# Kernel tuning notes

Hardware: AMD Instinct MI355X
Metric: run time of the kernel (lower is better)

Reference implementation:

```python
import jax, jax.numpy as jnp
import numpy as np

H = 12          # num_attention_heads
DH = 64         # attention_head_size
EPS = 1e-12     # F.normalize eps
MAX_LOG_SCALE = float(np.log(1.0 / 0.01))  # clamp max for logit_scale


def _l2norm(x):
    # F.normalize(x, dim=-1): x / max(||x||_2, eps)
    n = jnp.sqrt(jnp.sum(x * x, axis=-1, keepdims=True))
    return x / jnp.maximum(n, EPS)


def setup_inputs() -> dict:
    key = jax.random.key(0)
    ks = jax.random.split(key, 9)
    B, S, D = 4, 2048, 768
    sd = 1.0 / np.sqrt(D)
    inp = {
        "hidden_states": jax.random.normal(ks[0], (B, S, D), jnp.float32),
        "Wq": jax.random.normal(ks[1], (D, D), jnp.float32) * sd,
        "bq": jnp.zeros((D,), jnp.float32),
        "Wk": jax.random.normal(ks[2], (D, D), jnp.float32) * sd,
        "bk": jnp.zeros((D,), jnp.float32),
        "Wv": jax.random.normal(ks[3], (D, D), jnp.float32) * sd,
        "bv": jnp.zeros((D,), jnp.float32),
        "Wo": jax.random.normal(ks[4], (D, D), jnp.float32) * sd,
        "bo": jnp.zeros((D,), jnp.float32),
        "logit_scale": jnp.log(10.0 * jnp.ones((H, 1, 1), jnp.float32)),
    }
    return inp


def reference(hidden_states, Wq, bq, Wk, bk, Wv, bv, Wo, bo, logit_scale):
    B, S, D = hidden_states.shape
    # QKV projections (torch Linear: x @ W.T + b), split heads -> [B,H,S,DH]
    def proj(W, b):
        y = hidden_states @ W.T + b
        return y.reshape(B, S, H, DH).transpose(0, 2, 1, 3)
    q = proj(Wq, bq)
    k = proj(Wk, bk)
    v = proj(Wv, bv)
    # cosine-similarity scores scaled by clamped-exp per-head logit scale
    scale = jnp.exp(jnp.minimum(logit_scale, MAX_LOG_SCALE))  # [H,1,1]
    scores = jnp.einsum('bhqd,bhkd->bhqk', _l2norm(q), _l2norm(k)) * scale[None]
    probs = jax.nn.softmax(scores, axis=-1)
    ctx = jnp.einsum('bhqk,bhkd->bhqd', probs, v)
    ctx = ctx.transpose(0, 2, 1, 3).reshape(B, S, D)
    return ctx @ Wo.T + bo
```

## Files before the change

kernel.cpp:

```cpp
#include <hip/hip_runtime.h>
#include <math.h>

#define Hh 12
#define S_LEN 2048
#define D_MODEL 768
#define HD 64

static constexpr float MAXLS = 4.6051701859880914f;
static constexpr float LOG2E = 1.4426950408889634f;

typedef short bf16x8 __attribute__((ext_vector_type(8)));
typedef float f32x4  __attribute__((ext_vector_type(4)));
typedef float f32x16 __attribute__((ext_vector_type(16)));
typedef unsigned short u16x4 __attribute__((ext_vector_type(4)));
typedef unsigned short u16x8 __attribute__((ext_vector_type(8)));
typedef unsigned int u32x4 __attribute__((ext_vector_type(4)));

__device__ __forceinline__ unsigned short f2bf(float x) {
    unsigned int u = __builtin_bit_cast(unsigned int, x);
    unsigned int r = (u + 0x7FFF + ((u >> 16) & 1)) >> 16;
    return (unsigned short)r;
}

__device__ __forceinline__ unsigned int cvtpk(float a, float b) {
    unsigned int r;
    asm("v_cvt_pk_bf16_f32 %0, %1, %2" : "=v"(r) : "v"(a), "v"(b));
    return r;
}

__device__ __forceinline__ void gload16(const void* g, void* l) {
    __builtin_amdgcn_global_load_lds(
        (const __attribute__((address_space(1))) unsigned int*)g,
        (__attribute__((address_space(3))) unsigned int*)l, 16, 0, 0);
}

__global__ __launch_bounds__(256)
void convert_bf16(const float* __restrict__ hs,
                  const float* __restrict__ Wq, const float* __restrict__ Wk,
                  const float* __restrict__ Wv, const float* __restrict__ Wo,
                  unsigned short* __restrict__ hsb,
                  unsigned short* __restrict__ wqkvb,
                  unsigned short* __restrict__ wob)
{
    const long long N0 = 8192LL * 768;
    const long long NW = 768LL * 768;
    const long long e  = ((long long)blockIdx.x * 256 + threadIdx.x) * 8;
    const float* src; unsigned short* dst;
    if (e < N0) { src = hs + e; dst = hsb + e; }
    else if (e < N0 + 3*NW) {
        const long long r = e - N0;
        const int z = (int)(r / NW);
        src = (z == 0 ? Wq : z == 1 ? Wk : Wv) + (r - (long long)z * NW);
        dst = wqkvb + r;
    } else {
        const long long r = e - N0 - 3*NW;
        src = Wo + r; dst = wob + r;
    }
    const float4 f0 = *(const float4*)src;
    const float4 f1 = *(const float4*)(src + 4);
    u16x8 o;
    o[0]=f2bf(f0.x); o[1]=f2bf(f0.y); o[2]=f2bf(f0.z); o[3]=f2bf(f0.w);
    o[4]=f2bf(f1.x); o[5]=f2bf(f1.y); o[6]=f2bf(f1.z); o[7]=f2bf(f1.w);
    *(u16x8*)dst = o;
}

template<int MODE>
__global__ __launch_bounds__(256)
void gemm_bf16(const unsigned short* __restrict__ A,
               const unsigned short* __restrict__ Wt,
               const float* __restrict__ b0, const float* __restrict__ b1,
               const float* __restrict__ b2, const float* __restrict__ ls,
               unsigned short* __restrict__ qb, unsigned short* __restrict__ kb,
               unsigned short* __restrict__ vt, float* __restrict__ out)
{
    constexpr int K = 768;
    __shared__ char As[16384];
    __shared__ char Bs[16384];

    const int tid = threadIdx.x, w = tid >> 6, l = tid & 63;
    const int wr = w >> 1, wc = w & 1, hi = l >> 4, ll = l & 15;
    const int n0 = blockIdx.x * 128, m0 = blockIdx.y * 128;

    const int srow = l >> 3;
    const int sch  = (l & 7) ^ srow;
    const char* Ab = (const char*)(A  + (size_t)(m0 + w*32) * K) + srow * (K*2) + sch * 16;
    const char* Bb = (const char*)(Wt + (size_t)(n0 + w*32) * K) + srow * (K*2) + sch * 16;
    char* AsW = As + (w*32) * 128;
    char* BsW = Bs + (w*32) * 128;

    f32x4 acc[4][4];
    #pragma unroll
    for (int i = 0; i < 4; ++i)
        #pragma unroll
        for (int j = 0; j < 4; ++j) acc[i][j] = (f32x4){0.f,0.f,0.f,0.f};

    for (int kt = 0; kt < K/64; ++kt) {
        __syncthreads();
        #pragma unroll
        for (int s = 0; s < 4; ++s) {
            gload16(Ab + kt*128 + s*8*(K*2), AsW + s*1024);
            gload16(Bb + kt*128 + s*8*(K*2), BsW + s*1024);
        }
        __syncthreads();

        bf16x8 af[2][4], bf[2][4];
        #pragma unroll
        for (int kk = 0; kk < 2; ++kk) {
            const int pc = kk*4 + hi;
            #pragma unroll
            for (int i = 0; i < 4; ++i) {
                const int ra = wr*64 + i*16 + ll;
                af[kk][i] = *(const bf16x8*)(As + ra*128 + ((pc ^ (ra & 7)) << 4));
                const int rb = wc*64 + i*16 + ll;
                bf[kk][i] = *(const bf16x8*)(Bs + rb*128 + ((pc ^ (rb & 7)) << 4));
            }
        }
        #pragma unroll
        for (int kk = 0; kk < 2; ++kk)
            #pragma unroll
            for (int i = 0; i < 4; ++i)
                #pragma unroll
                for (int j = 0; j < 4; ++j)
                    acc[i][j] = __builtin_amdgcn_mfma_f32_16x16x32_bf16(af[kk][i], bf[kk][j], acc[i][j], 0, 0, 0);
    }

    if (MODE == 0) {
        const int z  = n0 / 768;
        const int nl = (n0 % 768) + wc*64;
        const int h  = nl >> 6;
        const int b  = m0 >> 11;
        const int s0 = (m0 & (S_LEN-1)) + wr*64;
        const float* bias = (z == 0) ? b0 : (z == 1) ? b1 : b2;
        float bj[4];
        #pragma unroll
        for (int j = 0; j < 4; ++j) bj[j] = bias[nl + j*16 + ll];

        if (z < 2) {
            const float sc = (z == 0) ? expf(fminf(ls[h], MAXLS)) * LOG2E : 1.0f;
            unsigned short* dst = (z == 0 ? qb : kb) + ((size_t)(b*Hh + h) * S_LEN) * HD;
            #pragma unroll
            for (int i = 0; i < 4; ++i) {
                float vv[4][4]; float ss[4] = {0.f, 0.f, 0.f, 0.f};
                #pragma unroll
                for (int r = 0; r < 4; ++r)
                    #pragma unroll
                    for (int j = 0; j < 4; ++j) {
                        const float x = acc[i][j][r] + bj[j];
                        vv[r][j] = x; ss[r] += x * x;
                    }
                #pragma unroll
                for (int mm = 1; mm < 16; mm <<= 1) {
                    ss[0] += __shfl_xor(ss[0], mm, 64);
                    ss[1] += __shfl_xor(ss[1], mm, 64);
                    ss[2] += __shfl_xor(ss[2], mm, 64);
                    ss[3] += __shfl_xor(ss[3], mm, 64);
                }
                #pragma unroll
                for (int r = 0; r < 4; ++r) {
                    const float inv = sc / fmaxf(sqrtf(ss[r]), 1e-12f);
                    const int s = s0 + i*16 + hi*4 + r;
                    u16x4 o;
                    #pragma unroll
                    for (int j = 0; j < 4; ++j) o[j] = f2bf(vv[r][j] * inv);
                    *(u16x4*)(dst + (size_t)s * HD + ll*4) = o;
                }
            }
        } else {
            const int hsw = ((hi & 1) << 1) | (hi >> 1);
            #pragma unroll
            for (int j = 0; j < 4; ++j) {
                const int d = (nl & 63) + j*16 + ll;
                #pragma unroll
                for (int i = 0; i < 4; ++i) {
                    const int s = s0 + i*16 + hsw*4;
                    u16x4 o;
                    #pragma unroll
                    for (int r = 0; r < 4; ++r) o[r] = f2bf(acc[i][j][r] + bj[j]);
                    *(u16x4*)(vt + ((size_t)(b*Hh + h) * HD + d) * S_LEN + s) = o;
                }
            }
        }
    } else {
        #pragma unroll
        for (int i = 0; i < 4; ++i)
            #pragma unroll
            for (int j = 0; j < 4; ++j) {
                const int n = n0 + wc*64 + j*16 + ll;
                const float bn = b0[n];
                #pragma unroll
                for (int r = 0; r < 4; ++r) {
                    const int m = m0 + wr*64 + i*16 + hi*4 + r;
                    out[(size_t)m * D_MODEL + n] = acc[i][j][r] + bn;
                }
            }
    }
}

__global__ __launch_bounds__(256)
void attn_mfma4(const char* __restrict__ qb_, const char* __restrict__ kb_,
                const char* __restrict__ vtb_,
                unsigned short* __restrict__ ctx)
{
    __shared__ char smem[32768];

    const int flat = blockIdx.x;
    const int xcd = flat & 7, ix = flat >> 3;
    const int bh = xcd * 6 + (ix >> 4);
    const int q0 = (ix & 15) * 128;
    const int b = bh / Hh, h = bh % Hh;

    const int tid = threadIdx.x, w = tid >> 6, l = tid & 63;
    const int lq = l & 31, g = l >> 5;

    const char* qg = qb_ + ((size_t)bh * S_LEN + q0 + w * 32) * 128;
    const char* kg = kb_ + (size_t)bh * S_LEN * 128 + (size_t)l * 128;
    const char* vg = vtb_ + (size_t)bh * HD * (S_LEN * 2) + (size_t)l * 4096;

    bf16x8 qf[4];
    #pragma unroll
    for (int s = 0; s < 4; ++s)
        qf[s] = *(const bf16x8*)(qg + lq * 128 + s * 32 + g * 16);

    const short oneb = (short)0x3F80;
    const bf16x8 onesf = {oneb, oneb, oneb, oneb, oneb, oneb, oneb, oneb};

    f32x16 acco0, acco1, accl;
    #pragma unroll
    for (int i = 0; i < 16; ++i) { acco0[i] = 0.f; acco1[i] = 0.f; accl[i] = 0.f; }

#define STAGE(buf, kt) do {                                                  \
        char* dstS = smem + ((buf) << 14);                                   \
        gload16(kg + (size_t)(kt) * 8192 + w * 16,        dstS + w * 1024);          \
        gload16(kg + (size_t)(kt) * 8192 + (w+4) * 16,    dstS + (w+4) * 1024);      \
        gload16(vg + (size_t)(kt) * 128 + w * 16,         dstS + 8192 + w * 1024);   \
        gload16(vg + (size_t)(kt) * 128 + (w+4) * 16,     dstS + 8192 + (w+4) * 1024); \
    } while (0)

    STAGE(0, 0);
    __syncthreads();
    int cur = 0;

    for (int kt = 0; kt < S_LEN / 64; ++kt) {
        if (kt < S_LEN / 64 - 1) STAGE(cur ^ 1, kt + 1);

        const char* Ks = smem + (cur << 14);
        const char* Vs = Ks + 8192;

        f32x16 sa0, sa1;
        #pragma unroll
        for (int i = 0; i < 16; ++i) { sa0[i] = 0.f; sa1[i] = 0.f; }

        __builtin_amdgcn_s_setprio(1);
        #pragma unroll
        for (int s = 0; s < 4; ++s) {
            const bf16x8 kf0 = *(const bf16x8*)(Ks + (2*s + g) * 1024 + lq * 16);
            sa0 = __builtin_amdgcn_mfma_f32_32x32x16_bf16(kf0, qf[s], sa0, 0, 0, 0);
            const bf16x8 kf1 = *(const bf16x8*)(Ks + (2*s + g) * 1024 + 512 + lq * 16);
            sa1 = __builtin_amdgcn_mfma_f32_32x32x16_bf16(kf1, qf[s], sa1, 0, 0, 0);
        }
        __builtin_amdgcn_s_setprio(0);

        #pragma unroll
        for (int t = 0; t < 4; ++t) {
            float p[8];
            #pragma unroll
            for (int e = 0; e < 8; ++e) {
                const float sv = (t & 2) ? sa1[8*(t&1) + e] : sa0[8*(t&1) + e];
                p[e] = __builtin_amdgcn_exp2f(sv);
            }
            u32x4 pu;
            pu[0] = cvtpk(p[0], p[1]);
            pu[1] = cvtpk(p[2], p[3]);
            pu[2] = cvtpk(p[4], p[5]);
            pu[3] = cvtpk(p[6], p[7]);
            const bf16x8 pa = __builtin_bit_cast(bf16x8, pu);

            __builtin_amdgcn_s_setprio(1);
            const bf16x8 vf0 = *(const bf16x8*)(Vs + (2*t + g) * 1024 + lq * 16);
            acco0 = __builtin_amdgcn_mfma_f32_32x32x16_bf16(pa, vf0, acco0, 0, 0, 0);
            const bf16x8 vf1 = *(const bf16x8*)(Vs + (2*t + g) * 1024 + 512 + lq * 16);
            acco1 = __builtin_amdgcn_mfma_f32_32x32x16_bf16(pa, vf1, acco1, 0, 0, 0);
            accl  = __builtin_amdgcn_mfma_f32_32x32x16_bf16(pa, onesf, accl, 0, 0, 0);
            __builtin_amdgcn_s_setprio(0);
        }

        __syncthreads();
        cur ^= 1;
    }
#undef STAGE

    #pragma unroll
    for (int r = 0; r < 16; ++r) {
        const int qrow = (r & 3) + 8 * (r >> 2) + 4 * g;
        const float inv = 1.0f / accl[r];
        unsigned short* crow = ctx + ((size_t)b * S_LEN + q0 + w * 32 + qrow) * D_MODEL + h * HD;
        crow[lq]      = f2bf(acco0[r] * inv);
        crow[32 + lq] = f2bf(acco1[r] * inv);
    }
}

extern "C" void kernel_launch(void* const* d_in, const int* in_sizes, int n_in,
                              void* d_out, int out_size, void* d_ws, size_t ws_size,
                              hipStream_t stream)
{
    const float* hs = (const float*)d_in[0];
    const float* Wq = (const float*)d_in[1];
    const float* bq = (const float*)d_in[2];
    const float* Wk = (const float*)d_in[3];
    const float* bk = (const float*)d_in[4];
    const float* Wv = (const float*)d_in[5];
    const float* bv = (const float*)d_in[6];
    const float* Wo = (const float*)d_in[7];
    const float* bo = (const float*)d_in[8];
    const float* ls = (const float*)d_in[9];
    float* out = (float*)d_out;

    const int B = 4;
    const size_t nHS = 8192ULL * 768;
    const size_t nW  = 768ULL * 768;
    const size_t nPB = (size_t)B * Hh * S_LEN * HD;

    unsigned short* hsb   = (unsigned short*)d_ws;
    unsigned short* wqkvb = hsb + nHS;
    unsigned short* wob   = wqkvb + 3 * nW;
    unsigned short* qbuf  = wob + nW;
    unsigned short* kbuf  = qbuf + nPB;
    unsigned short* vtb   = kbuf + nPB;
    unsigned short* cbuf  = vtb + nPB;

    hipLaunchKernelGGL(convert_bf16, dim3(4224), dim3(256), 0, stream,
                       hs, Wq, Wk, Wv, Wo, hsb, wqkvb, wob);

    hipLaunchKernelGGL((gemm_bf16<0>), dim3(2304/128, 8192/128), dim3(256), 0, stream,
                       hsb, wqkvb, bq, bk, bv, ls, qbuf, kbuf, vtb, nullptr);

    hipLaunchKernelGGL(attn_mfma4, dim3((S_LEN/128) * B * Hh), dim3(256), 0, stream,
                       (const char*)qbuf, (const char*)kbuf, (const char*)vtb, cbuf);

    hipLaunchKernelGGL((gemm_bf16<1>), dim3(768/128, 8192/128), dim3(256), 0, stream,
                       cbuf, wob, bo, nullptr, nullptr, nullptr,
                       nullptr, nullptr, nullptr, out);
}
```

Before: 229.2 us.

## Pipeline attention QK ahead of PV, remap GEMM blocks per XCD, stage V-transpose through LDS

The attention kernel now uses a triple-buffered LDS ring and computes the QK scores for the next tile before the softmax and PV of the current tile, so matrix work can overlap exp and loads. Its launch bounds now request 4 blocks per CU. The GEMMs get a flattened grid with an XCD-aware block remap. The output projection uses a narrower 64-column tile, which gives more blocks. The V-transpose epilogue in the QKV GEMM goes through LDS so it can issue coalesced 16-byte row stores instead of scattered 8-byte stores. These changes add register pressure and LDS use in attention, plus an extra barrier in the GEMM epilogue.

```diff
diff --git a/kernel.cpp b/kernel.cpp
--- a/kernel.cpp
+++ b/kernel.cpp
@@ -64,7 +64,7 @@
     *(u16x8*)dst = o;
 }
 
-template<int MODE>
+template<int MODE, int BN, int NWGX>
 __global__ __launch_bounds__(256)
 void gemm_bf16(const unsigned short* __restrict__ A,
                const unsigned short* __restrict__ Wt,
@@ -73,37 +73,44 @@
                unsigned short* __restrict__ qb, unsigned short* __restrict__ kb,
                unsigned short* __restrict__ vt, float* __restrict__ out)
 {
-    constexpr int K = 768;
+    constexpr int K  = 768;
+    constexpr int JW = BN / 32;
     __shared__ char As[16384];
-    __shared__ char Bs[16384];
+    __shared__ char Bs[BN * 128];
+
+    constexpr int CPX = (NWGX * 64) / 8;
+    const int bid = blockIdx.x;
+    const int wg  = (bid & 7) * CPX + (bid >> 3);
+    const int n0  = (wg % NWGX) * BN;
+    const int m0  = (wg / NWGX) * 128;
 
     const int tid = threadIdx.x, w = tid >> 6, l = tid & 63;
     const int wr = w >> 1, wc = w & 1, hi = l >> 4, ll = l & 15;
-    const int n0 = blockIdx.x * 128, m0 = blockIdx.y * 128;
 
     const int srow = l >> 3;
     const int sch  = (l & 7) ^ srow;
     const char* Ab = (const char*)(A  + (size_t)(m0 + w*32) * K) + srow * (K*2) + sch * 16;
-    const char* Bb = (const char*)(Wt + (size_t)(n0 + w*32) * K) + srow * (K*2) + sch * 16;
+    const char* Bb = (const char*)(Wt + (size_t)(n0 + w*(BN/4)) * K) + srow * (K*2) + sch * 16;
     char* AsW = As + (w*32) * 128;
-    char* BsW = Bs + (w*32) * 128;
-
-    f32x4 acc[4][4];
+    char* BsW = Bs + (w*(BN/4)) * 128;
+
+    f32x4 acc[4][JW];
     #pragma unroll
     for (int i = 0; i < 4; ++i)
         #pragma unroll
-        for (int j = 0; j < 4; ++j) acc[i][j] = (f32x4){0.f,0.f,0.f,0.f};
+        for (int j = 0; j < JW; ++j) acc[i][j] = (f32x4){0.f,0.f,0.f,0.f};
 
     for (int kt = 0; kt < K/64; ++kt) {
         __syncthreads();
         #pragma unroll
-        for (int s = 0; s < 4; ++s) {
+        for (int s = 0; s < 4; ++s)
             gload16(Ab + kt*128 + s*8*(K*2), AsW + s*1024);
+        #pragma unroll
+        for (int s = 0; s < JW; ++s)
             gload16(Bb + kt*128 + s*8*(K*2), BsW + s*1024);
-        }
         __syncthreads();
 
-        bf16x8 af[2][4], bf[2][4];
+        bf16x8 af[2][4], bf[2][JW];
         #pragma unroll
         for (int kk = 0; kk < 2; ++kk) {
             const int pc = kk*4 + hi;
@@ -111,8 +118,11 @@
             for (int i = 0; i < 4; ++i) {
                 const int ra = wr*64 + i*16 + ll;
                 af[kk][i] = *(const bf16x8*)(As + ra*128 + ((pc ^ (ra & 7)) << 4));
-                const int rb = wc*64 + i*16 + ll;
-                bf[kk][i] = *(const bf16x8*)(Bs + rb*128 + ((pc ^ (rb & 7)) << 4));
+            }
+            #pragma unroll
+            for (int j = 0; j < JW; ++j) {
+                const int rb = wc*(BN/2) + j*16 + ll;
+                bf[kk][j] = *(const bf16x8*)(Bs + rb*128 + ((pc ^ (rb & 7)) << 4));
             }
         }
         #pragma unroll
@@ -120,7 +130,7 @@
             #pragma unroll
             for (int i = 0; i < 4; ++i)
                 #pragma unroll
-                for (int j = 0; j < 4; ++j)
+                for (int j = 0; j < JW; ++j)
                     acc[i][j] = __builtin_amdgcn_mfma_f32_16x16x32_bf16(af[kk][i], bf[kk][j], acc[i][j], 0, 0, 0);
     }
 
@@ -166,17 +176,32 @@
                 }
             }
         } else {
-            const int hsw = ((hi & 1) << 1) | (hi >> 1);
+            __syncthreads();
+            char* T = (w < 2 ? As : Bs) + (w & 1) * 8192;
+            const int ch_add = hi & 1;
+            const int half8  = hi >> 1;
             #pragma unroll
             for (int j = 0; j < 4; ++j) {
-                const int d = (nl & 63) + j*16 + ll;
+                const int d = j*16 + ll;
                 #pragma unroll
                 for (int i = 0; i < 4; ++i) {
-                    const int s = s0 + i*16 + hsw*4;
                     u16x4 o;
                     #pragma unroll
                     for (int r = 0; r < 4; ++r) o[r] = f2bf(acc[i][j][r] + bj[j]);
-                    *(u16x4*)(vt + ((size_t)(b*Hh + h) * HD + d) * S_LEN + s) = o;
+                    const int byteoff = d*128 + (((i*2 + ch_add) ^ (d & 7)) << 4) + half8*8;
+                    *(u16x4*)(T + byteoff) = o;
+                }
+            }
+            const int dl = l >> 2;
+            #pragma unroll
+            for (int dp = 0; dp < 4; ++dp) {
+                const int d = dp*16 + dl;
+                unsigned short* vrow = vt + ((size_t)(b*Hh + h) * HD + d) * S_LEN + s0;
+                #pragma unroll
+                for (int rep = 0; rep < 2; ++rep) {
+                    const int c = (l & 3) + rep*4;
+                    const u16x8 vv = *(const u16x8*)(T + d*128 + ((c ^ (d & 7)) << 4));
+                    *(u16x8*)(vrow + c*8) = vv;
                 }
             }
         }
@@ -184,8 +209,8 @@
         #pragma unroll
         for (int i = 0; i < 4; ++i)
             #pragma unroll
-            for (int j = 0; j < 4; ++j) {
-                const int n = n0 + wc*64 + j*16 + ll;
+            for (int j = 0; j < JW; ++j) {
+                const int n = n0 + wc*(BN/2) + j*16 + ll;
                 const float bn = b0[n];
                 #pragma unroll
                 for (int r = 0; r < 4; ++r) {
@@ -196,12 +221,13 @@
     }
 }
 
-__global__ __launch_bounds__(256)
-void attn_mfma4(const char* __restrict__ qb_, const char* __restrict__ kb_,
+__global__ __launch_bounds__(256, 4)
+void attn_mfma5(const char* __restrict__ qb_, const char* __restrict__ kb_,
                 const char* __restrict__ vtb_,
                 unsigned short* __restrict__ ctx)
 {
-    __shared__ char smem[32768];
+    __shared__ char smem[49152];
+    constexpr int NT = S_LEN / 64;
 
     const int flat = blockIdx.x;
     const int xcd = flat & 7, ix = flat >> 3;
@@ -228,44 +254,33 @@
     #pragma unroll
     for (int i = 0; i < 16; ++i) { acco0[i] = 0.f; acco1[i] = 0.f; accl[i] = 0.f; }
 
-#define STAGE(buf, kt) do {                                                  \
-        char* dstS = smem + ((buf) << 14);                                   \
+#define STAGE(bi, kt) do {                                                   \
+        char* dstS = smem + ((bi) << 14);                                    \
         gload16(kg + (size_t)(kt) * 8192 + w * 16,        dstS + w * 1024);          \
         gload16(kg + (size_t)(kt) * 8192 + (w+4) * 16,    dstS + (w+4) * 1024);      \
         gload16(vg + (size_t)(kt) * 128 + w * 16,         dstS + 8192 + w * 1024);   \
         gload16(vg + (size_t)(kt) * 128 + (w+4) * 16,     dstS + 8192 + (w+4) * 1024); \
     } while (0)
 
-    STAGE(0, 0);
-    __syncthreads();
-    int cur = 0;
-
-    for (int kt = 0; kt < S_LEN / 64; ++kt) {
-        if (kt < S_LEN / 64 - 1) STAGE(cur ^ 1, kt + 1);
-
-        const char* Ks = smem + (cur << 14);
-        const char* Vs = Ks + 8192;
-
-        f32x16 sa0, sa1;
-        #pragma unroll
-        for (int i = 0; i < 16; ++i) { sa0[i] = 0.f; sa1[i] = 0.f; }
-
+    auto qk = [&](const char* Ks, f32x16& o0, f32x16& o1) {
         __builtin_amdgcn_s_setprio(1);
         #pragma unroll
         for (int s = 0; s < 4; ++s) {
             const bf16x8 kf0 = *(const bf16x8*)(Ks + (2*s + g) * 1024 + lq * 16);
-            sa0 = __builtin_amdgcn_mfma_f32_32x32x16_bf16(kf0, qf[s], sa0, 0, 0, 0);
+            o0 = __builtin_amdgcn_mfma_f32_32x32x16_bf16(kf0, qf[s], o0, 0, 0, 0);
             const bf16x8 kf1 = *(const bf16x8*)(Ks + (2*s + g) * 1024 + 512 + lq * 16);
-            sa1 = __builtin_amdgcn_mfma_f32_32x32x16_bf16(kf1, qf[s], sa1, 0, 0, 0);
+            o1 = __builtin_amdgcn_mfma_f32_32x32x16_bf16(kf1, qf[s], o1, 0, 0, 0);
         }
         __builtin_amdgcn_s_setprio(0);
-
+    };
+
+    auto softmax_pv = [&](const f32x16& s0v, const f32x16& s1v, const char* Vs) {
         #pragma unroll
         for (int t = 0; t < 4; ++t) {
             float p[8];
             #pragma unroll
             for (int e = 0; e < 8; ++e) {
-                const float sv = (t & 2) ? sa1[8*(t&1) + e] : sa0[8*(t&1) + e];
+                const float sv = (t & 2) ? s1v[8*(t&1) + e] : s0v[8*(t&1) + e];
                 p[e] = __builtin_amdgcn_exp2f(sv);
             }
             u32x4 pu;
@@ -283,10 +298,31 @@
             accl  = __builtin_amdgcn_mfma_f32_32x32x16_bf16(pa, onesf, accl, 0, 0, 0);
             __builtin_amdgcn_s_setprio(0);
         }
-
+    };
+
+    STAGE(0, 0);
+    __syncthreads();
+    STAGE(1, 1);
+    f32x16 sa0c, sa1c;
+    #pragma unroll
+    for (int i = 0; i < 16; ++i) { sa0c[i] = 0.f; sa1c[i] = 0.f; }
+    qk(smem, sa0c, sa1c);
+    __syncthreads();
+
+    int bc = 0, bn = 1, bs = 2;
+    #pragma unroll 3
+    for (int kt = 0; kt < NT - 1; ++kt) {
+        if (kt + 2 < NT) STAGE(bs, kt + 2);
+        f32x16 sa0n, sa1n;
+        #pragma unroll
+        for (int i = 0; i < 16; ++i) { sa0n[i] = 0.f; sa1n[i] = 0.f; }
+        qk(smem + (bn << 14), sa0n, sa1n);
+        softmax_pv(sa0c, sa1c, smem + (bc << 14) + 8192);
         __syncthreads();
-        cur ^= 1;
-    }
+        sa0c = sa0n; sa1c = sa1n;
+        const int t0 = bc; bc = bn; bn = bs; bs = t0;
+    }
+    softmax_pv(sa0c, sa1c, smem + (bc << 14) + 8192);
 #undef STAGE
 
     #pragma unroll
@@ -331,13 +367,13 @@
     hipLaunchKernelGGL(convert_bf16, dim3(4224), dim3(256), 0, stream,
                        hs, Wq, Wk, Wv, Wo, hsb, wqkvb, wob);
 
-    hipLaunchKernelGGL((gemm_bf16<0>), dim3(2304/128, 8192/128), dim3(256), 0, stream,
+    hipLaunchKernelGGL((gemm_bf16<0, 128, 18>), dim3(18 * 64), dim3(256), 0, stream,
                        hsb, wqkvb, bq, bk, bv, ls, qbuf, kbuf, vtb, nullptr);
 
-    hipLaunchKernelGGL(attn_mfma4, dim3((S_LEN/128) * B * Hh), dim3(256), 0, stream,
+    hipLaunchKernelGGL(attn_mfma5, dim3((S_LEN/128) * B * Hh), dim3(256), 0, stream,
                        (const char*)qbuf, (const char*)kbuf, (const char*)vtb, cbuf);
 
-    hipLaunchKernelGGL((gemm_bf16<1>), dim3(768/128, 8192/128), dim3(256), 0, stream,
+    hipLaunchKernelGGL((gemm_bf16<1, 64, 12>), dim3(12 * 64), dim3(256), 0, stream,
                        cbuf, wob, bo, nullptr, nullptr, nullptr,
                        nullptr, nullptr, nullptr, out);
 }
```

After: 214.8 us. 1.07x faster.
